# Kernel optimization log

Measured on AMD Instinct MI355X. Metric: run time of the kernel, lower is better.

Reference implementation:

```python
import jax, jax.numpy as jnp
import numpy as np

M = 8192      # nodes
D = 128       # feature dim
DEG = 32      # neighbors per node


def setup_inputs() -> dict:
    key = jax.random.key(0)
    ks = jax.random.split(key, 6)
    z = jax.random.normal(ks[0], (M, D), dtype=jnp.float32)
    # deterministic, duplicate-free edge list: node i -> (i+1..i+DEG) mod M
    src = jnp.repeat(jnp.arange(M, dtype=jnp.int64), DEG)
    dst = (src + jnp.tile(jnp.arange(1, DEG + 1, dtype=jnp.int64), M)) % M
    edge_index = jnp.stack([src, dst], axis=0)  # [2, M*DEG]
    s = 1.0 / np.sqrt(D)
    Wg = jax.random.normal(ks[1], (D, D), dtype=jnp.float32) * s
    Wc = jax.random.normal(ks[2], (D, D), dtype=jnp.float32) * s
    Wq = jax.random.normal(ks[3], (D, D), dtype=jnp.float32) * s
    Wk = jax.random.normal(ks[4], (D, D), dtype=jnp.float32) * s
    a = jax.random.normal(ks[5], (2 * D,), dtype=jnp.float32)
    return {"z": z, "edge_index": edge_index, "Wg": Wg, "Wc": Wc,
            "Wq": Wq, "Wk": Wk, "a": a}


def reference(z, edge_index, Wg, Wc, Wq, Wk, a):
    m, d = z.shape
    wg = z @ Wg.T                              # [m, d]
    src, dst = edge_index[0], edge_index[1]
    a_src, a_dst = a[:d], a[d:]
    # per-edge score: leaky_relu(a . [wg[i], wg[j]]) = leaky_relu(a1.wg[i] + a2.wg[j])
    scores = jax.nn.leaky_relu((wg @ a_src)[src] + (wg @ a_dst)[dst])  # [E]
    # softmax over each source node's neighbors (segment softmax)
    smax = jax.ops.segment_max(scores, src, num_segments=m)
    ex = jnp.exp(scores - smax[src])
    denom = jax.ops.segment_sum(ex, src, num_segments=m)
    alpha = ex / denom[src]                    # [E]
    # scatter-aggregate: local[i] = sum_j alpha_ij * wg[j]
    local = jax.ops.segment_sum(alpha[:, None] * wg[dst], src, num_segments=m)
    # dense global attention branch
    q = z @ Wq.T
    k = z @ Wk.T
    beta = jax.nn.softmax(q @ k.T / jnp.sqrt(jnp.float32(d)), axis=-1)  # [m, m]
    global_msg = beta @ (z @ Wc.T)
    return jax.nn.leaky_relu(local + global_msg + z)
```

## Files before the change

### kernel.cpp

```cpp
#include <hip/hip_runtime.h>

#define MM 8192
#define DD 128
#define DEG 32
#define KSPLIT 8

typedef __attribute__((ext_vector_type(8))) _Float16 h8;
typedef __attribute__((ext_vector_type(4))) float f4;
typedef __attribute__((ext_vector_type(4))) unsigned int u4;
typedef __attribute__((ext_vector_type(4))) short s4;

__device__ __forceinline__ unsigned short f2h(float f) {
  _Float16 h = (_Float16)f;
  return __builtin_bit_cast(unsigned short, h);
}

__device__ __forceinline__ void lds_dma16(const unsigned short* gptr, unsigned short* lptr) {
  __builtin_amdgcn_global_load_lds(
      (const __attribute__((address_space(1))) unsigned int*)gptr,
      (__attribute__((address_space(3))) unsigned int*)lptr, 16, 0, 0);
}

__global__ __launch_bounds__(256) void proj_kernel(
    const float* __restrict__ z, const float* __restrict__ Wg,
    const float* __restrict__ Wc, const float* __restrict__ Wq,
    const float* __restrict__ Wk, const float* __restrict__ a,
    float* __restrict__ wg, unsigned short* __restrict__ qb,
    unsigned short* __restrict__ kb, unsigned short* __restrict__ ct,
    float* __restrict__ sg, float* __restrict__ sd)
{
  __shared__ unsigned short zt[64 * 136];
  __shared__ unsigned short wt[128 * 136];
  const int mode = blockIdx.y;
  const float* __restrict__ W = (mode == 0) ? Wg : (mode == 1) ? Wq : (mode == 2) ? Wk : Wc;
  const int r0 = blockIdx.x * 64;
  const int tid = threadIdx.x;

  #pragma unroll
  for (int it = 0; it < 8; ++it) {
    int id = tid + it * 256, row = id >> 5, c4 = (id & 31) * 4;
    f4 v = *(const f4*)(z + (r0 + row) * DD + c4);
    s4 sv = {(short)f2h(v.x), (short)f2h(v.y), (short)f2h(v.z), (short)f2h(v.w)};
    *(s4*)&zt[row * 136 + c4] = sv;
  }
  #pragma unroll
  for (int it = 0; it < 16; ++it) {
    int id = tid + it * 256, row = id >> 5, c4 = (id & 31) * 4;
    f4 v = *(const f4*)(W + row * DD + c4);
    s4 sv = {(short)f2h(v.x), (short)f2h(v.y), (short)f2h(v.z), (short)f2h(v.w)};
    *(s4*)&wt[row * 136 + c4] = sv;
  }
  __syncthreads();

  const int lane = tid & 63, w = tid >> 6, n = lane & 15, quad = lane >> 4;
  h8 afr[4];
  #pragma unroll
  for (int kt = 0; kt < 4; ++kt)
    afr[kt] = *(const h8*)&zt[(16 * w + n) * 136 + kt * 32 + quad * 8];

  f4 acc[8];
  const f4 fzero = {0.f, 0.f, 0.f, 0.f};
  #pragma unroll
  for (int nt = 0; nt < 8; ++nt) {
    f4 c = fzero;
    #pragma unroll
    for (int kt = 0; kt < 4; ++kt) {
      h8 b = *(const h8*)&wt[(16 * nt + n) * 136 + kt * 32 + quad * 8];
      c = __builtin_amdgcn_mfma_f32_16x16x32_f16(afr[kt], b, c, 0, 0, 0);
    }
    acc[nt] = c;
  }

  if (mode == 0) {
    #pragma unroll
    for (int nt = 0; nt < 8; ++nt)
      #pragma unroll
      for (int r = 0; r < 4; ++r)
        wg[(r0 + 16 * w + quad * 4 + r) * DD + 16 * nt + n] = acc[nt][r];
    float av[8], bv[8];
    #pragma unroll
    for (int nt = 0; nt < 8; ++nt) { av[nt] = a[16 * nt + n]; bv[nt] = a[DD + 16 * nt + n]; }
    #pragma unroll
    for (int r = 0; r < 4; ++r) {
      float s1 = 0.f, s2 = 0.f;
      #pragma unroll
      for (int nt = 0; nt < 8; ++nt) { s1 += acc[nt][r] * av[nt]; s2 += acc[nt][r] * bv[nt]; }
      s1 += __shfl_xor(s1, 1); s1 += __shfl_xor(s1, 2); s1 += __shfl_xor(s1, 4); s1 += __shfl_xor(s1, 8);
      s2 += __shfl_xor(s2, 1); s2 += __shfl_xor(s2, 2); s2 += __shfl_xor(s2, 4); s2 += __shfl_xor(s2, 8);
      if (n == 0) {
        int g = r0 + 16 * w + quad * 4 + r;
        sg[g] = s1; sd[g] = s2;
      }
    }
  } else if (mode == 1) {
    const float qscale = 0.08838834764831845f;
    #pragma unroll
    for (int nt = 0; nt < 8; ++nt)
      #pragma unroll
      for (int r = 0; r < 4; ++r)
        qb[(r0 + 16 * w + quad * 4 + r) * DD + 16 * nt + n] = f2h(acc[nt][r] * qscale);
  } else if (mode == 2) {
    #pragma unroll
    for (int nt = 0; nt < 8; ++nt)
      #pragma unroll
      for (int r = 0; r < 4; ++r)
        kb[(r0 + 16 * w + quad * 4 + r) * DD + 16 * nt + n] = f2h(acc[nt][r]);
  } else {
    __syncthreads();
    #pragma unroll
    for (int nt = 0; nt < 8; ++nt)
      #pragma unroll
      for (int r = 0; r < 4; ++r)
        wt[(16 * nt + n) * 80 + 16 * w + quad * 4 + r] = f2h(acc[nt][r]);
    __syncthreads();
    #pragma unroll
    for (int it = 0; it < 4; ++it) {
      int idx = tid + it * 256, d = idx >> 3, c8 = (idx & 7) * 8;
      u4 v = *(const u4*)&wt[d * 80 + c8];
      *(u4*)(ct + (size_t)d * MM + r0 + c8) = v;
    }
  }
}

__global__ __launch_bounds__(128) void edge_kernel(
    const int* __restrict__ ei, const float* __restrict__ wg,
    const float* __restrict__ sg, const float* __restrict__ sd,
    float* __restrict__ loc)
{
  __shared__ float alpha_s[DEG];
  __shared__ int dst_s[DEG];
  const int i = blockIdx.x, tid = threadIdx.x;
  if (tid < DEG) {
    int dstj = ei[MM * DEG + i * DEG + tid];
    float s = sg[i] + sd[dstj];
    s = s > 0.f ? s : 0.01f * s;
    float mx = s;
    #pragma unroll
    for (int off = 1; off < DEG; off <<= 1) mx = fmaxf(mx, __shfl_xor(mx, off));
    float p = __expf(s - mx);
    float sum = p;
    #pragma unroll
    for (int off = 1; off < DEG; off <<= 1) sum += __shfl_xor(sum, off);
    alpha_s[tid] = p / sum;
    dst_s[tid] = dstj;
  }
  __syncthreads();
  float accum = 0.f;
  #pragma unroll 8
  for (int j = 0; j < DEG; ++j)
    accum += alpha_s[j] * wg[(size_t)dst_s[j] * DD + tid];
  loc[(size_t)i * DD + tid] = accum;
}

__global__ __launch_bounds__(256, 2) void flash_kernel(
    const unsigned short* __restrict__ qb, const unsigned short* __restrict__ kb,
    const unsigned short* __restrict__ ct, unsigned short* __restrict__ Opart,
    float* __restrict__ Lpart)
{
  __shared__ unsigned short sh[25600];
  const int bx = blockIdx.x, ck = blockIdx.y;
  const int tid = threadIdx.x, lane = tid & 63, w = tid >> 6;
  const int n = lane & 15, quad = lane >> 4;
  const int ln = lane & 15, lq = lane >> 4;
  const int qr0 = bx * 128;

  #pragma unroll
  for (int it = 0; it < 8; ++it)
    lds_dma16(qb + (qr0 + it * 16 + ln) * DD + w * 32 + lq * 8,
              &sh[(it * 256 + tid) * 8]);
  __syncthreads();
  h8 aq[2][4];
  #pragma unroll
  for (int mt = 0; mt < 2; ++mt)
    #pragma unroll
    for (int kt = 0; kt < 4; ++kt)
      aq[mt][kt] = *(const h8*)&sh[((w * 2 + mt) * 4 + kt) * 512 + lane * 8];

  f4 acc_o[2][8];
  const f4 fzero = {0.f, 0.f, 0.f, 0.f};
  #pragma unroll
  for (int mt = 0; mt < 2; ++mt)
    #pragma unroll
    for (int dt = 0; dt < 8; ++dt) acc_o[mt][dt] = fzero;
  float l_r[2][4] = {{0.f, 0.f, 0.f, 0.f}, {0.f, 0.f, 0.f, 0.f}};
  const int pbase = 16384 + w * 2304;

  for (int t = 0; t < 16; ++t) {
    const int j0 = ck * 1024 + t * 64;
    __syncthreads();
    #pragma unroll
    for (int it = 0; it < 4; ++it)
      lds_dma16(kb + (j0 + 4 * ln + it) * DD + w * 32 + lq * 8,
                &sh[(it * 256 + tid) * 8]);
    #pragma unroll
    for (int it = 0; it < 4; ++it) {
      int dt = it * 2 + (w >> 1), k2 = w & 1;
      lds_dma16(ct + (size_t)(16 * dt + ln) * MM + j0 + k2 * 32 + lq * 8,
                &sh[8192 + (it * 256 + tid) * 8]);
    }
    __syncthreads();

    f4 accs[2][4];
    #pragma unroll
    for (int mt = 0; mt < 2; ++mt)
      #pragma unroll
      for (int nt = 0; nt < 4; ++nt) accs[mt][nt] = fzero;
    #pragma unroll
    for (int nt = 0; nt < 4; ++nt) {
      #pragma unroll
      for (int kt = 0; kt < 4; ++kt) {
        h8 bk = *(const h8*)&sh[nt * 2048 + kt * 512 + lane * 8];
        accs[0][nt] = __builtin_amdgcn_mfma_f32_16x16x32_f16(aq[0][kt], bk, accs[0][nt], 0, 0, 0);
        accs[1][nt] = __builtin_amdgcn_mfma_f32_16x16x32_f16(aq[1][kt], bk, accs[1][nt], 0, 0, 0);
      }
    }

    #pragma unroll
    for (int mt = 0; mt < 2; ++mt)
      #pragma unroll
      for (int r = 0; r < 4; ++r) {
        float p0 = __expf(fminf(accs[mt][0][r], 10.f));
        float p1 = __expf(fminf(accs[mt][1][r], 10.f));
        float p2 = __expf(fminf(accs[mt][2][r], 10.f));
        float p3 = __expf(fminf(accs[mt][3][r], 10.f));
        l_r[mt][r] += p0 + p1 + p2 + p3;
        unsigned int lo = ((unsigned int)f2h(p1) << 16) | f2h(p0);
        unsigned int hi = ((unsigned int)f2h(p3) << 16) | f2h(p2);
        uint2 pv; pv.x = lo; pv.y = hi;
        *(uint2*)&sh[pbase + (mt * 16 + quad * 4 + r) * 72 + n * 4] = pv;
      }

    h8 ap[2][2];
    #pragma unroll
    for (int mt = 0; mt < 2; ++mt)
      #pragma unroll
      for (int k2 = 0; k2 < 2; ++k2)
        ap[mt][k2] = *(const h8*)&sh[pbase + (mt * 16 + n) * 72 + k2 * 32 + quad * 8];
    #pragma unroll
    for (int dt = 0; dt < 8; ++dt) {
      #pragma unroll
      for (int k2 = 0; k2 < 2; ++k2) {
        h8 bv = *(const h8*)&sh[8192 + dt * 1024 + k2 * 512 + lane * 8];
        acc_o[0][dt] = __builtin_amdgcn_mfma_f32_16x16x32_f16(ap[0][k2], bv, acc_o[0][dt], 0, 0, 0);
        acc_o[1][dt] = __builtin_amdgcn_mfma_f32_16x16x32_f16(ap[1][k2], bv, acc_o[1][dt], 0, 0, 0);
      }
    }
  }

  #pragma unroll
  for (int mt = 0; mt < 2; ++mt)
    #pragma unroll
    for (int r = 0; r < 4; ++r) {
      float lv = l_r[mt][r];
      lv += __shfl_xor(lv, 1); lv += __shfl_xor(lv, 2);
      lv += __shfl_xor(lv, 4); lv += __shfl_xor(lv, 8);
      int g = qr0 + w * 32 + mt * 16 + quad * 4 + r;
      if (n == 0) Lpart[ck * MM + g] = lv;
      #pragma unroll
      for (int dt = 0; dt < 8; ++dt)
        Opart[((size_t)ck * MM + g) * DD + 16 * dt + n] = f2h(acc_o[mt][dt][r]);
    }
}

__global__ __launch_bounds__(256) void merge_kernel(
    const unsigned short* __restrict__ Opart, const float* __restrict__ Lpart,
    const float* __restrict__ loc, const float* __restrict__ z,
    float* __restrict__ out)
{
  int gid = blockIdx.x * 256 + threadIdx.x;
  int g = gid >> 4, c8 = (gid & 15) * 8;
  float l = 0.f;
  float o[8] = {0.f, 0.f, 0.f, 0.f, 0.f, 0.f, 0.f, 0.f};
  #pragma unroll
  for (int ck = 0; ck < KSPLIT; ++ck) {
    l += Lpart[ck * MM + g];
    h8 v = *(const h8*)(Opart + ((size_t)ck * MM + g) * DD + c8);
    #pragma unroll
    for (int j = 0; j < 8; ++j) o[j] += (float)v[j];
  }
  float inv = 1.0f / l;
  const float* lp = loc + (size_t)g * DD + c8;
  const float* zp = z + (size_t)g * DD + c8;
  float* op = out + (size_t)g * DD + c8;
  #pragma unroll
  for (int j = 0; j < 8; ++j) {
    float r = o[j] * inv + lp[j] + zp[j];
    op[j] = r > 0.f ? r : 0.01f * r;
  }
}

extern "C" void kernel_launch(void* const* d_in, const int* in_sizes, int n_in,
                              void* d_out, int out_size, void* d_ws, size_t ws_size,
                              hipStream_t stream) {
  const float* z  = (const float*)d_in[0];
  const int*   ei = (const int*)d_in[1];
  const float* Wg = (const float*)d_in[2];
  const float* Wc = (const float*)d_in[3];
  const float* Wq = (const float*)d_in[4];
  const float* Wk = (const float*)d_in[5];
  const float* a  = (const float*)d_in[6];
  float* out = (float*)d_out;
  char* ws = (char*)d_ws;

  float*          wg    = (float*)(ws + 0);
  unsigned short* qb    = (unsigned short*)(ws + (4 << 20));
  unsigned short* kb    = (unsigned short*)(ws + (6 << 20));
  unsigned short* ct    = (unsigned short*)(ws + (8 << 20));
  float*          sg    = (float*)(ws + (10 << 20));
  float*          sd    = (float*)(ws + (10 << 20) + (64 << 10));
  float*          loc   = (float*)(ws + (11 << 20));
  unsigned short* Opart = (unsigned short*)(ws + (15 << 20));
  float*          Lpart = (float*)(ws + (31 << 20));

  proj_kernel<<<dim3(128, 4), 256, 0, stream>>>(z, Wg, Wc, Wq, Wk, a, wg, qb, kb, ct, sg, sd);
  edge_kernel<<<8192, 128, 0, stream>>>(ei, wg, sg, sd, loc);
  flash_kernel<<<dim3(64, KSPLIT), 256, 0, stream>>>(qb, kb, ct, Opart, Lpart);
  merge_kernel<<<512, 256, 0, stream>>>(Opart, Lpart, loc, z, out);
}
```

Baseline: 139.5 us.

## Double-buffer K/V tiles in LDS for the flash attention kernel

The flash kernel now keeps two LDS buffers for the K and V^T tiles. It prefetches tile t+1 with global_load_lds while computing on tile t, which removes one barrier per iteration and lets memory latency overlap with MFMA work. The per-wave P staging area is cut to 16 rows and reused for both row tiles, so the larger footprint (about 73 KB per block) still allows two blocks per CU. This relies on the barrier waiting for the outstanding LDS DMA, and the higher LDS use could limit occupancy.

```diff
diff --git a/kernel.cpp b/kernel.cpp
--- a/kernel.cpp
+++ b/kernel.cpp
@@ -157,11 +157,11 @@
     const unsigned short* __restrict__ ct, unsigned short* __restrict__ Opart,
     float* __restrict__ Lpart)
 {
-  __shared__ unsigned short sh[25600];
+  __shared__ unsigned short sh[37376];
   const int bx = blockIdx.x, ck = blockIdx.y;
   const int tid = threadIdx.x, lane = tid & 63, w = tid >> 6;
   const int n = lane & 15, quad = lane >> 4;
-  const int ln = lane & 15, lq = lane >> 4;
+  const int ln = n, lq = quad;
   const int qr0 = bx * 128;
 
   #pragma unroll
@@ -175,6 +175,17 @@
     #pragma unroll
     for (int kt = 0; kt < 4; ++kt)
       aq[mt][kt] = *(const h8*)&sh[((w * 2 + mt) * 4 + kt) * 512 + lane * 8];
+  __syncthreads();
+
+  const unsigned short* kp = kb + (size_t)(ck * 1024 + 4 * ln) * DD + w * 32 + lq * 8;
+  const unsigned short* vp = ct + (size_t)(16 * (w >> 1) + ln) * MM + ck * 1024 + (w & 1) * 32 + lq * 8;
+
+  #pragma unroll
+  for (int it = 0; it < 4; ++it)
+    lds_dma16(kp + it * DD, &sh[(it * 256 + tid) * 8]);
+  #pragma unroll
+  for (int it = 0; it < 4; ++it)
+    lds_dma16(vp + (size_t)it * 32 * MM, &sh[8192 + (it * 256 + tid) * 8]);
 
   f4 acc_o[2][8];
   const f4 fzero = {0.f, 0.f, 0.f, 0.f};
@@ -183,22 +194,23 @@
     #pragma unroll
     for (int dt = 0; dt < 8; ++dt) acc_o[mt][dt] = fzero;
   float l_r[2][4] = {{0.f, 0.f, 0.f, 0.f}, {0.f, 0.f, 0.f, 0.f}};
-  const int pbase = 16384 + w * 2304;
+  const int pbase = 32768 + w * 1152;
 
   for (int t = 0; t < 16; ++t) {
-    const int j0 = ck * 1024 + t * 64;
     __syncthreads();
-    #pragma unroll
-    for (int it = 0; it < 4; ++it)
-      lds_dma16(kb + (j0 + 4 * ln + it) * DD + w * 32 + lq * 8,
-                &sh[(it * 256 + tid) * 8]);
-    #pragma unroll
-    for (int it = 0; it < 4; ++it) {
-      int dt = it * 2 + (w >> 1), k2 = w & 1;
-      lds_dma16(ct + (size_t)(16 * dt + ln) * MM + j0 + k2 * 32 + lq * 8,
-                &sh[8192 + (it * 256 + tid) * 8]);
-    }
-    __syncthreads();
+    const int cur = (t & 1) * 16384;
+
+    if (t < 15) {
+      const int nb = ((t + 1) & 1) * 16384;
+      const unsigned short* kpn = kp + (size_t)(t + 1) * 64 * DD;
+      const unsigned short* vpn = vp + (t + 1) * 64;
+      #pragma unroll
+      for (int it = 0; it < 4; ++it)
+        lds_dma16(kpn + it * DD, &sh[nb + (it * 256 + tid) * 8]);
+      #pragma unroll
+      for (int it = 0; it < 4; ++it)
+        lds_dma16(vpn + (size_t)it * 32 * MM, &sh[nb + 8192 + (it * 256 + tid) * 8]);
+    }
 
     f4 accs[2][4];
     #pragma unroll
@@ -209,14 +221,15 @@
     for (int nt = 0; nt < 4; ++nt) {
       #pragma unroll
       for (int kt = 0; kt < 4; ++kt) {
-        h8 bk = *(const h8*)&sh[nt * 2048 + kt * 512 + lane * 8];
+        h8 bk = *(const h8*)&sh[cur + nt * 2048 + kt * 512 + lane * 8];
         accs[0][nt] = __builtin_amdgcn_mfma_f32_16x16x32_f16(aq[0][kt], bk, accs[0][nt], 0, 0, 0);
         accs[1][nt] = __builtin_amdgcn_mfma_f32_16x16x32_f16(aq[1][kt], bk, accs[1][nt], 0, 0, 0);
       }
     }
 
-    #pragma unroll
-    for (int mt = 0; mt < 2; ++mt)
+    h8 ap[2][2];
+    #pragma unroll
+    for (int mt = 0; mt < 2; ++mt) {
       #pragma unroll
       for (int r = 0; r < 4; ++r) {
         float p0 = __expf(fminf(accs[mt][0][r], 10.f));
@@ -227,20 +240,17 @@
         unsigned int lo = ((unsigned int)f2h(p1) << 16) | f2h(p0);
         unsigned int hi = ((unsigned int)f2h(p3) << 16) | f2h(p2);
         uint2 pv; pv.x = lo; pv.y = hi;
-        *(uint2*)&sh[pbase + (mt * 16 + quad * 4 + r) * 72 + n * 4] = pv;
+        *(uint2*)&sh[pbase + (quad * 4 + r) * 72 + n * 4] = pv;
       }
-
-    h8 ap[2][2];
-    #pragma unroll
-    for (int mt = 0; mt < 2; ++mt)
-      #pragma unroll
-      for (int k2 = 0; k2 < 2; ++k2)
-        ap[mt][k2] = *(const h8*)&sh[pbase + (mt * 16 + n) * 72 + k2 * 32 + quad * 8];
+      ap[mt][0] = *(const h8*)&sh[pbase + n * 72 + quad * 8];
+      ap[mt][1] = *(const h8*)&sh[pbase + n * 72 + 32 + quad * 8];
+    }
+
     #pragma unroll
     for (int dt = 0; dt < 8; ++dt) {
       #pragma unroll
       for (int k2 = 0; k2 < 2; ++k2) {
-        h8 bv = *(const h8*)&sh[8192 + dt * 1024 + k2 * 512 + lane * 8];
+        h8 bv = *(const h8*)&sh[cur + 8192 + dt * 1024 + k2 * 512 + lane * 8];
         acc_o[0][dt] = __builtin_amdgcn_mfma_f32_16x16x32_f16(ap[0][k2], bv, acc_o[0][dt], 0, 0, 0);
         acc_o[1][dt] = __builtin_amdgcn_mfma_f32_16x16x32_f16(ap[1][k2], bv, acc_o[1][dt], 0, 0, 0);
       }
```

Result: faster. 135.8 us (-2.7%).

## Double-buffer flash attention tiles, shrink query tile, fuse edge aggregation into merge

Applied to the files above, without the earlier changes.

The flash kernel now processes 64 query rows per block (16 per wave) with 32-key tiles, loaded into double-buffered LDS by asynchronous DMA so the next tile streams in while the current one is computed. Q fragments are read straight from global memory into registers. Occupancy is raised to 4 blocks per CU and the grid doubles to 128x8. The edge softmax/aggregation kernel is folded into the merge kernel, which removes one launch and the round trip of the loc buffer through memory. In exchange, each K/V tile is reused by fewer query rows, so more K/V is fetched overall, and the merge step now does per-element scalar loads instead of vectorised ones.

```diff
diff --git a/kernel.cpp b/kernel.cpp
--- a/kernel.cpp
+++ b/kernel.cpp
@@ -122,171 +122,132 @@
   }
 }
 
-__global__ __launch_bounds__(128) void edge_kernel(
-    const int* __restrict__ ei, const float* __restrict__ wg,
-    const float* __restrict__ sg, const float* __restrict__ sd,
-    float* __restrict__ loc)
-{
-  __shared__ float alpha_s[DEG];
-  __shared__ int dst_s[DEG];
-  const int i = blockIdx.x, tid = threadIdx.x;
-  if (tid < DEG) {
-    int dstj = ei[MM * DEG + i * DEG + tid];
-    float s = sg[i] + sd[dstj];
-    s = s > 0.f ? s : 0.01f * s;
-    float mx = s;
-    #pragma unroll
-    for (int off = 1; off < DEG; off <<= 1) mx = fmaxf(mx, __shfl_xor(mx, off));
-    float p = __expf(s - mx);
-    float sum = p;
-    #pragma unroll
-    for (int off = 1; off < DEG; off <<= 1) sum += __shfl_xor(sum, off);
-    alpha_s[tid] = p / sum;
-    dst_s[tid] = dstj;
-  }
-  __syncthreads();
-  float accum = 0.f;
-  #pragma unroll 8
-  for (int j = 0; j < DEG; ++j)
-    accum += alpha_s[j] * wg[(size_t)dst_s[j] * DD + tid];
-  loc[(size_t)i * DD + tid] = accum;
-}
-
-__global__ __launch_bounds__(256, 2) void flash_kernel(
+__global__ __launch_bounds__(256, 4) void flash_kernel(
     const unsigned short* __restrict__ qb, const unsigned short* __restrict__ kb,
     const unsigned short* __restrict__ ct, unsigned short* __restrict__ Opart,
     float* __restrict__ Lpart)
 {
-  __shared__ unsigned short sh[25600];
+  __shared__ unsigned short sh[18944];
   const int bx = blockIdx.x, ck = blockIdx.y;
   const int tid = threadIdx.x, lane = tid & 63, w = tid >> 6;
   const int n = lane & 15, quad = lane >> 4;
-  const int ln = lane & 15, lq = lane >> 4;
-  const int qr0 = bx * 128;
-
-  #pragma unroll
-  for (int it = 0; it < 8; ++it)
-    lds_dma16(qb + (qr0 + it * 16 + ln) * DD + w * 32 + lq * 8,
-              &sh[(it * 256 + tid) * 8]);
+  const int qr0 = bx * 64;
+
+  h8 aq[4];
+  #pragma unroll
+  for (int kt = 0; kt < 4; ++kt)
+    aq[kt] = *(const h8*)(qb + (qr0 + 16 * w + n) * DD + kt * 32 + quad * 8);
+
+  const unsigned short* kp = kb + (size_t)(ck * 1024 + 2 * n) * DD + w * 32 + quad * 8;
+  const unsigned short* vp0 = ct + (size_t)(16 * (0 + w) + n) * MM + ck * 1024 + quad * 8;
+  const unsigned short* vp1 = ct + (size_t)(16 * (4 + w) + n) * MM + ck * 1024 + quad * 8;
+
+  lds_dma16(kp, &sh[tid * 8]);
+  lds_dma16(kp + DD, &sh[(256 + tid) * 8]);
+  lds_dma16(vp0, &sh[8192 + tid * 8]);
+  lds_dma16(vp1, &sh[8192 + (256 + tid) * 8]);
+
+  f4 acc_o[8];
+  const f4 fzero = {0.f, 0.f, 0.f, 0.f};
+  #pragma unroll
+  for (int dt = 0; dt < 8; ++dt) acc_o[dt] = fzero;
+  float l_r[4] = {0.f, 0.f, 0.f, 0.f};
+  const int pb = 16384 + w * 640;
+
+  for (int t = 0; t < 32; ++t) {
+    asm volatile("s_waitcnt vmcnt(0)" ::: "memory");
+    __syncthreads();
+    const int cur = (t & 1) * 4096;
+
+    if (t < 31) {
+      const int nb = ((t + 1) & 1) * 4096;
+      const unsigned short* kpn = kp + (size_t)(t + 1) * 32 * DD;
+      lds_dma16(kpn, &sh[nb + tid * 8]);
+      lds_dma16(kpn + DD, &sh[nb + (256 + tid) * 8]);
+      lds_dma16(vp0 + (t + 1) * 32, &sh[8192 + nb + tid * 8]);
+      lds_dma16(vp1 + (t + 1) * 32, &sh[8192 + nb + (256 + tid) * 8]);
+    }
+
+    f4 a0 = fzero, a1 = fzero;
+    #pragma unroll
+    for (int kt = 0; kt < 4; ++kt) {
+      h8 bk0 = *(const h8*)&sh[cur + (kt * 64 + lane) * 8];
+      h8 bk1 = *(const h8*)&sh[cur + ((4 + kt) * 64 + lane) * 8];
+      a0 = __builtin_amdgcn_mfma_f32_16x16x32_f16(aq[kt], bk0, a0, 0, 0, 0);
+      a1 = __builtin_amdgcn_mfma_f32_16x16x32_f16(aq[kt], bk1, a1, 0, 0, 0);
+    }
+
+    #pragma unroll
+    for (int r = 0; r < 4; ++r) {
+      float p0 = __expf(fminf(a0[r], 10.f));
+      float p1 = __expf(fminf(a1[r], 10.f));
+      l_r[r] += p0 + p1;
+      unsigned int pv = ((unsigned int)f2h(p1) << 16) | f2h(p0);
+      *(unsigned int*)&sh[pb + (quad * 4 + r) * 40 + 2 * n] = pv;
+    }
+    h8 ap = *(const h8*)&sh[pb + n * 40 + quad * 8];
+
+    #pragma unroll
+    for (int dt = 0; dt < 8; ++dt) {
+      h8 bv = *(const h8*)&sh[cur + 8192 + (dt * 64 + lane) * 8];
+      acc_o[dt] = __builtin_amdgcn_mfma_f32_16x16x32_f16(ap, bv, acc_o[dt], 0, 0, 0);
+    }
+  }
+
+  #pragma unroll
+  for (int r = 0; r < 4; ++r) {
+    float lv = l_r[r];
+    lv += __shfl_xor(lv, 1); lv += __shfl_xor(lv, 2);
+    lv += __shfl_xor(lv, 4); lv += __shfl_xor(lv, 8);
+    int g = qr0 + 16 * w + quad * 4 + r;
+    if (n == 0) Lpart[ck * MM + g] = lv;
+    #pragma unroll
+    for (int dt = 0; dt < 8; ++dt)
+      Opart[((size_t)ck * MM + g) * DD + 16 * dt + n] = f2h(acc_o[dt][r]);
+  }
+}
+
+__global__ __launch_bounds__(256) void merge_kernel(
+    const int* __restrict__ ei, const float* __restrict__ wg,
+    const float* __restrict__ sg, const float* __restrict__ sd,
+    const unsigned short* __restrict__ Opart, const float* __restrict__ Lpart,
+    const float* __restrict__ z, float* __restrict__ out)
+{
+  __shared__ float alpha_s[2][DEG];
+  __shared__ int dst_s[2][DEG];
+  const int tid = threadIdx.x, nl = tid >> 7, d = tid & 127;
+  const int i = blockIdx.x * 2 + nl;
+
+  if (d < DEG) {
+    int dstj = ei[MM * DEG + i * DEG + d];
+    float s = sg[i] + sd[dstj];
+    s = s > 0.f ? s : 0.01f * s;
+    float mx = s;
+    #pragma unroll
+    for (int off = 1; off < DEG; off <<= 1) mx = fmaxf(mx, __shfl_xor(mx, off));
+    float p = __expf(s - mx);
+    float sum = p;
+    #pragma unroll
+    for (int off = 1; off < DEG; off <<= 1) sum += __shfl_xor(sum, off);
+    alpha_s[nl][d] = p / sum;
+    dst_s[nl][d] = dstj;
+  }
   __syncthreads();
-  h8 aq[2][4];
-  #pragma unroll
-  for (int mt = 0; mt < 2; ++mt)
-    #pragma unroll
-    for (int kt = 0; kt < 4; ++kt)
-      aq[mt][kt] = *(const h8*)&sh[((w * 2 + mt) * 4 + kt) * 512 + lane * 8];
-
-  f4 acc_o[2][8];
-  const f4 fzero = {0.f, 0.f, 0.f, 0.f};
-  #pragma unroll
-  for (int mt = 0; mt < 2; ++mt)
-    #pragma unroll
-    for (int dt = 0; dt < 8; ++dt) acc_o[mt][dt] = fzero;
-  float l_r[2][4] = {{0.f, 0.f, 0.f, 0.f}, {0.f, 0.f, 0.f, 0.f}};
-  const int pbase = 16384 + w * 2304;
-
-  for (int t = 0; t < 16; ++t) {
-    const int j0 = ck * 1024 + t * 64;
-    __syncthreads();
-    #pragma unroll
-    for (int it = 0; it < 4; ++it)
-      lds_dma16(kb + (j0 + 4 * ln + it) * DD + w * 32 + lq * 8,
-                &sh[(it * 256 + tid) * 8]);
-    #pragma unroll
-    for (int it = 0; it < 4; ++it) {
-      int dt = it * 2 + (w >> 1), k2 = w & 1;
-      lds_dma16(ct + (size_t)(16 * dt + ln) * MM + j0 + k2 * 32 + lq * 8,
-                &sh[8192 + (it * 256 + tid) * 8]);
-    }
-    __syncthreads();
-
-    f4 accs[2][4];
-    #pragma unroll
-    for (int mt = 0; mt < 2; ++mt)
-      #pragma unroll
-      for (int nt = 0; nt < 4; ++nt) accs[mt][nt] = fzero;
-    #pragma unroll
-    for (int nt = 0; nt < 4; ++nt) {
-      #pragma unroll
-      for (int kt = 0; kt < 4; ++kt) {
-        h8 bk = *(const h8*)&sh[nt * 2048 + kt * 512 + lane * 8];
-        accs[0][nt] = __builtin_amdgcn_mfma_f32_16x16x32_f16(aq[0][kt], bk, accs[0][nt], 0, 0, 0);
-        accs[1][nt] = __builtin_amdgcn_mfma_f32_16x16x32_f16(aq[1][kt], bk, accs[1][nt], 0, 0, 0);
-      }
-    }
-
-    #pragma unroll
-    for (int mt = 0; mt < 2; ++mt)
-      #pragma unroll
-      for (int r = 0; r < 4; ++r) {
-        float p0 = __expf(fminf(accs[mt][0][r], 10.f));
-        float p1 = __expf(fminf(accs[mt][1][r], 10.f));
-        float p2 = __expf(fminf(accs[mt][2][r], 10.f));
-        float p3 = __expf(fminf(accs[mt][3][r], 10.f));
-        l_r[mt][r] += p0 + p1 + p2 + p3;
-        unsigned int lo = ((unsigned int)f2h(p1) << 16) | f2h(p0);
-        unsigned int hi = ((unsigned int)f2h(p3) << 16) | f2h(p2);
-        uint2 pv; pv.x = lo; pv.y = hi;
-        *(uint2*)&sh[pbase + (mt * 16 + quad * 4 + r) * 72 + n * 4] = pv;
-      }
-
-    h8 ap[2][2];
-    #pragma unroll
-    for (int mt = 0; mt < 2; ++mt)
-      #pragma unroll
-      for (int k2 = 0; k2 < 2; ++k2)
-        ap[mt][k2] = *(const h8*)&sh[pbase + (mt * 16 + n) * 72 + k2 * 32 + quad * 8];
-    #pragma unroll
-    for (int dt = 0; dt < 8; ++dt) {
-      #pragma unroll
-      for (int k2 = 0; k2 < 2; ++k2) {
-        h8 bv = *(const h8*)&sh[8192 + dt * 1024 + k2 * 512 + lane * 8];
-        acc_o[0][dt] = __builtin_amdgcn_mfma_f32_16x16x32_f16(ap[0][k2], bv, acc_o[0][dt], 0, 0, 0);
-        acc_o[1][dt] = __builtin_amdgcn_mfma_f32_16x16x32_f16(ap[1][k2], bv, acc_o[1][dt], 0, 0, 0);
-      }
-    }
-  }
-
-  #pragma unroll
-  for (int mt = 0; mt < 2; ++mt)
-    #pragma unroll
-    for (int r = 0; r < 4; ++r) {
-      float lv = l_r[mt][r];
-      lv += __shfl_xor(lv, 1); lv += __shfl_xor(lv, 2);
-      lv += __shfl_xor(lv, 4); lv += __shfl_xor(lv, 8);
-      int g = qr0 + w * 32 + mt * 16 + quad * 4 + r;
-      if (n == 0) Lpart[ck * MM + g] = lv;
-      #pragma unroll
-      for (int dt = 0; dt < 8; ++dt)
-        Opart[((size_t)ck * MM + g) * DD + 16 * dt + n] = f2h(acc_o[mt][dt][r]);
-    }
-}
-
-__global__ __launch_bounds__(256) void merge_kernel(
-    const unsigned short* __restrict__ Opart, const float* __restrict__ Lpart,
-    const float* __restrict__ loc, const float* __restrict__ z,
-    float* __restrict__ out)
-{
-  int gid = blockIdx.x * 256 + threadIdx.x;
-  int g = gid >> 4, c8 = (gid & 15) * 8;
-  float l = 0.f;
-  float o[8] = {0.f, 0.f, 0.f, 0.f, 0.f, 0.f, 0.f, 0.f};
+
+  float accum = 0.f;
+  #pragma unroll 8
+  for (int j = 0; j < DEG; ++j)
+    accum += alpha_s[nl][j] * wg[(size_t)dst_s[nl][j] * DD + d];
+
+  float l = 0.f, o = 0.f;
   #pragma unroll
   for (int ck = 0; ck < KSPLIT; ++ck) {
-    l += Lpart[ck * MM + g];
-    h8 v = *(const h8*)(Opart + ((size_t)ck * MM + g) * DD + c8);
-    #pragma unroll
-    for (int j = 0; j < 8; ++j) o[j] += (float)v[j];
-  }
-  float inv = 1.0f / l;
-  const float* lp = loc + (size_t)g * DD + c8;
-  const float* zp = z + (size_t)g * DD + c8;
-  float* op = out + (size_t)g * DD + c8;
-  #pragma unroll
-  for (int j = 0; j < 8; ++j) {
-    float r = o[j] * inv + lp[j] + zp[j];
-    op[j] = r > 0.f ? r : 0.01f * r;
-  }
+    l += Lpart[ck * MM + i];
+    unsigned short u = Opart[((size_t)ck * MM + i) * DD + d];
+    o += (float)__builtin_bit_cast(_Float16, u);
+  }
+  float r = o / l + accum + z[(size_t)i * DD + d];
+  out[(size_t)i * DD + d] = r > 0.f ? r : 0.01f * r;
 }
 
 extern "C" void kernel_launch(void* const* d_in, const int* in_sizes, int n_in,
@@ -308,12 +269,10 @@
   unsigned short* ct    = (unsigned short*)(ws + (8 << 20));
   float*          sg    = (float*)(ws + (10 << 20));
   float*          sd    = (float*)(ws + (10 << 20) + (64 << 10));
-  float*          loc   = (float*)(ws + (11 << 20));
   unsigned short* Opart = (unsigned short*)(ws + (15 << 20));
   float*          Lpart = (float*)(ws + (31 << 20));
 
   proj_kernel<<<dim3(128, 4), 256, 0, stream>>>(z, Wg, Wc, Wq, Wk, a, wg, qb, kb, ct, sg, sd);
-  edge_kernel<<<8192, 128, 0, stream>>>(ei, wg, sg, sd, loc);
-  flash_kernel<<<dim3(64, KSPLIT), 256, 0, stream>>>(qb, kb, ct, Opart, Lpart);
-  merge_kernel<<<512, 256, 0, stream>>>(Opart, Lpart, loc, z, out);
-}
+  flash_kernel<<<dim3(128, KSPLIT), 256, 0, stream>>>(qb, kb, ct, Opart, Lpart);
+  merge_kernel<<<4096, 256, 0, stream>>>(ei, wg, sg, sd, Opart, Lpart, z, out);
+}
```

Result: slower. 150.9 us (+8.2%).
